# Kernel tuning notes

Hardware: AMD Instinct MI355X
Metric: run time of the kernel (lower is better)

The kernel has to match this reference:

```python
import jax, jax.numpy as jnp
import numpy as np

N = 100000
E = 1600000
IN_F = 256
OUT_F = 128
ALPHA = 0.2  # LeakyReLU negative slope


def setup_inputs() -> dict:
    key = jax.random.key(0)
    k_x, k_e, k_w, k_al, k_ar = jax.random.split(key, 5)
    x = jax.random.normal(k_x, (N, IN_F), dtype=jnp.float32)
    edge_index = jax.random.randint(k_e, (2, E), 0, N, dtype=jnp.int64)
    # xavier_uniform with gain=1.414
    gain = 1.414
    lim_w = gain * np.sqrt(6.0 / (IN_F + OUT_F))
    W = jax.random.uniform(k_w, (IN_F, OUT_F), dtype=jnp.float32, minval=-lim_w, maxval=lim_w)
    lim_a = gain * np.sqrt(6.0 / (OUT_F + 1))
    a_left = jax.random.uniform(k_al, (OUT_F, 1), dtype=jnp.float32, minval=-lim_a, maxval=lim_a)
    a_right = jax.random.uniform(k_ar, (OUT_F, 1), dtype=jnp.float32, minval=-lim_a, maxval=lim_a)
    return {"x": x, "edge_index": edge_index, "W": W, "a_left": a_left, "a_right": a_right}


def reference(x, edge_index, W, a_left, a_right):
    src = edge_index[0]  # destination of aggregation (rows of adj)
    dst = edge_index[1]  # neighbor being attended to
    Wh = x @ W                              # [N, out_f]
    e_left = (Wh @ a_left)[:, 0]            # [N]
    e_right = (Wh @ a_right)[:, 0]          # [N]
    e = e_left[src] + e_right[dst]          # [E]
    e = jnp.where(e > 0, e, ALPHA * e)      # LeakyReLU
    # segment softmax over edges grouped by src node
    e_max = jax.ops.segment_max(e, src, num_segments=N)          # [N]
    e_exp = jnp.exp(e - e_max[src])                               # [E]
    e_sum = jax.ops.segment_sum(e_exp, src, num_segments=N)       # [N]
    alpha = e_exp / (e_sum[src] + 1e-9)                           # [E]
    messages = alpha[:, None] * Wh[dst]                           # [E, out_f]
    output = jax.ops.segment_sum(messages, src, num_segments=N)   # [N, out_f]
    return jax.nn.relu(output)
```

## Files before the change

### kernel.cpp

```cpp
#include <hip/hip_runtime.h>
#include <cstdint>
#include <cstddef>

static constexpr int IN_F  = 256;
static constexpr int OUT_F = 128;
#define ALPHA_SLOPE 0.2f
#define NB 256
#define BUCK_SH 7
#define CAP 6144

typedef __attribute__((ext_vector_type(8))) short short8;
typedef __attribute__((ext_vector_type(4))) float f32x4;
union ABFrag { uint32_t u[4]; short8 v; };

__device__ __forceinline__ uint32_t pack_bf2(float lo, float hi) {
    uint32_t ul = __float_as_uint(lo), uh = __float_as_uint(hi);
    uint32_t rl = (ul + 0x7fffu + ((ul >> 16) & 1u)) >> 16;
    uint32_t rh = (uh + 0x7fffu + ((uh >> 16) & 1u)) & 0xffff0000u;
    return rl | rh;
}
__device__ __forceinline__ uint32_t cvtpk_bf2(float lo, float hi) {
    uint32_t r;
    asm("v_cvt_pk_bf16_f32 %0, %1, %2" : "=v"(r) : "v"(lo), "v"(hi));
    return r;
}
__device__ __forceinline__ float blo(uint32_t w) { return __uint_as_float(w << 16); }
__device__ __forceinline__ float bhi(uint32_t w) { return __uint_as_float(w & 0xffff0000u); }

#define RL_F(x, l) __uint_as_float(__builtin_amdgcn_readlane(__float_as_uint(x), (l)))
#define RL_I(x, l) __builtin_amdgcn_readlane((x), (l))

__device__ __forceinline__ int edge_at(const void* ei, int idx, int is64) {
    return is64 ? (int)((const long long*)ei)[idx] : ((const int*)ei)[idx];
}

__global__ __launch_bounds__(256) void prep_hist_kernel(
    const float* __restrict__ W, const float* __restrict__ aL,
    const float* __restrict__ aR, const void* __restrict__ EI,
    int E, int nbuk, uint32_t* __restrict__ WtH,
    float* __restrict__ waL, float* __restrict__ waR, int* __restrict__ C)
{
    if (blockIdx.x < 64) {
        int dd = blockIdx.x * 256 + threadIdx.x;
        int n  = dd >> 7;
        int kd = (dd & 127) ^ ((n & 7) << 2);
        int k  = kd * 2;
        WtH[dd] = pack_bf2(W[(size_t)k * OUT_F + n], W[(size_t)(k + 1) * OUT_F + n]);
        return;
    }
    if (blockIdx.x == 64) {
        int k = threadIdx.x;
        const float* wr = W + (size_t)k * OUT_F;
        float sl = 0.f, sr = 0.f;
        for (int j = 0; j < OUT_F; j++) {
            float wv = wr[j];
            sl = fmaf(wv, aL[j], sl);
            sr = fmaf(wv, aR[j], sr);
        }
        waL[k] = sl; waR[k] = sr;
        return;
    }
    __shared__ int h[800];
    __shared__ int det;
    if (threadIdx.x == 0) det = 0;
    for (int b = threadIdx.x; b < nbuk; b += 256) h[b] = 0;
    __syncthreads();
    {
        const unsigned* eu = (const unsigned*)EI;
        int nz = 0;
        for (int i = threadIdx.x; i < 1024; i += 256)
            if (eu[2 * i + 1] != 0u) nz++;
        if (nz) atomicAdd(&det, 1);
    }
    __syncthreads();
    const int is64 = (det == 0);
    const int bid = blockIdx.x - 65;
    int chunk = (E + NB - 1) / NB;
    int start = bid * chunk;
    int end = min(start + chunk, E);
    for (int i = start + threadIdx.x; i < end; i += 256) {
        int s = edge_at(EI, i, is64);
        atomicAdd(&h[s >> BUCK_SH], 1);
    }
    __syncthreads();
    for (int b = threadIdx.x; b < nbuk; b += 256)
        C[b * NB + bid] = h[b];
}

__global__ __launch_bounds__(256) void scan1_kernel(const int* __restrict__ counts,
                                                    int* __restrict__ offsets,
                                                    int* __restrict__ partials, int N) {
    __shared__ int wt[4];
    int gid = blockIdx.x * 256 + threadIdx.x;
    const int lane = threadIdx.x & 63, wave = threadIdx.x >> 6;
    int c = (gid < N) ? counts[gid] : 0;
    int incl = c;
#pragma unroll
    for (int o = 1; o < 64; o <<= 1) {
        int v = __shfl_up(incl, o);
        if (lane >= o) incl += v;
    }
    if (lane == 63) wt[wave] = incl;
    __syncthreads();
    int woff = 0;
    for (int w = 0; w < wave; w++) woff += wt[w];
    if (gid < N) offsets[gid] = woff + incl - c;
    if (threadIdx.x == 0) partials[blockIdx.x] = wt[0] + wt[1] + wt[2] + wt[3];
}

__global__ __launch_bounds__(256) void scan2_kernel(int* data, int n) {
    __shared__ int wt[4];
    __shared__ int carry_s;
    if (threadIdx.x == 0) carry_s = 0;
    __syncthreads();
    const int lane = threadIdx.x & 63, wave = threadIdx.x >> 6;
    for (int base = 0; base < n; base += 256) {
        int i = base + threadIdx.x;
        int c = (i < n) ? data[i] : 0;
        int incl = c;
#pragma unroll
        for (int o = 1; o < 64; o <<= 1) {
            int v = __shfl_up(incl, o);
            if (lane >= o) incl += v;
        }
        if (lane == 63) wt[wave] = incl;
        __syncthreads();
        int woff = 0;
        for (int w = 0; w < wave; w++) woff += wt[w];
        int total = wt[0] + wt[1] + wt[2] + wt[3];
        int carry = carry_s;
        __syncthreads();
        if (i < n) data[i] = carry + woff + incl - c;
        if (threadIdx.x == 0) carry_s = carry + total;
        __syncthreads();
    }
}

__global__ __launch_bounds__(512, 4) void gemm_scatter_kernel(
    const float* __restrict__ X, const uint32_t* __restrict__ WtH,
    const float* __restrict__ waL, const float* __restrict__ waR,
    uint32_t* __restrict__ Whh, float* __restrict__ el, float* __restrict__ er,
    int M, const void* __restrict__ EI, int E, int nbuk,
    const int* __restrict__ Cx, const int* __restrict__ T,
    uint32_t* __restrict__ entries, int GB)
{
    __shared__ uint32_t ldsW[16384];
    __shared__ int cur[800];
    __shared__ int det;
    const int tid = threadIdx.x;

    if (blockIdx.x >= GB) {
        if (tid == 0) det = 0;
        for (int b = tid; b < nbuk; b += 512) cur[b] = 0;
        __syncthreads();
        {
            const unsigned* eu = (const unsigned*)EI;
            int nz = 0;
            for (int i = tid; i < 1024; i += 512)
                if (eu[2 * i + 1] != 0u) nz++;
            if (nz) atomicAdd(&det, 1);
        }
        __syncthreads();
        const int is64 = (det == 0);
        const int bid = blockIdx.x - GB;
        int chunk = (E + NB - 1) / NB;
        int start = bid * chunk;
        int end = min(start + chunk, E);
        for (int i = start + tid; i < end; i += 512) {
            int s = edge_at(EI, i, is64);
            int d = edge_at(EI, E + i, is64);
            int b = s >> BUCK_SH;
            int pos = T[b] + Cx[b * NB + bid] + atomicAdd(&cur[b], 1);
            entries[pos] = ((uint32_t)(s & 127) << 17) | (uint32_t)d;
        }
        return;
    }

    const int w = tid >> 6, l = tid & 63;
    const int c = l & 15, kg = l >> 4;
    const int swz = (c & 7) << 2;

    {
        const uint4* src = (const uint4*)WtH;
        uint4* dst = (uint4*)ldsW;
#pragma unroll
        for (int i = 0; i < 8; i++)
            dst[tid + i * 512] = src[tid + i * 512];
    }

    const int bm = blockIdx.x * 128;
    const int myrow = w * 16 + c;
    const int grow = min(bm + myrow, M - 1);
    const bool rv = (bm + myrow) < M;
    const float* xp = X + (size_t)grow * IN_F + kg * 8;

    float4 xv[16];
#pragma unroll
    for (int ks = 0; ks < 8; ks++) {
        xv[2 * ks]     = *(const float4*)(xp + ks * 32);
        xv[2 * ks + 1] = *(const float4*)(xp + ks * 32 + 4);
    }

    f32x4 acc[8];
#pragma unroll
    for (int j = 0; j < 8; j++) acc[j] = (f32x4){0.f, 0.f, 0.f, 0.f};
    float sl = 0.f, sr = 0.f;

    __syncthreads();

#pragma unroll
    for (int ks = 0; ks < 8; ks++) {
        float4 xa = xv[2 * ks], xb = xv[2 * ks + 1];
        const float* wlp = waL + ks * 32 + kg * 8;
        const float* wrp = waR + ks * 32 + kg * 8;
        float4 l0 = *(const float4*)wlp, l1 = *(const float4*)(wlp + 4);
        float4 r0 = *(const float4*)wrp, r1 = *(const float4*)(wrp + 4);
        sl = fmaf(xa.x, l0.x, sl); sl = fmaf(xa.y, l0.y, sl);
        sl = fmaf(xa.z, l0.z, sl); sl = fmaf(xa.w, l0.w, sl);
        sl = fmaf(xb.x, l1.x, sl); sl = fmaf(xb.y, l1.y, sl);
        sl = fmaf(xb.z, l1.z, sl); sl = fmaf(xb.w, l1.w, sl);
        sr = fmaf(xa.x, r0.x, sr); sr = fmaf(xa.y, r0.y, sr);
        sr = fmaf(xa.z, r0.z, sr); sr = fmaf(xa.w, r0.w, sr);
        sr = fmaf(xb.x, r1.x, sr); sr = fmaf(xb.y, r1.y, sr);
        sr = fmaf(xb.z, r1.z, sr); sr = fmaf(xb.w, r1.w, sr);
        ABFrag a;
        a.u[0] = cvtpk_bf2(xa.x, xa.y); a.u[1] = cvtpk_bf2(xa.z, xa.w);
        a.u[2] = cvtpk_bf2(xb.x, xb.y); a.u[3] = cvtpk_bf2(xb.z, xb.w);
        const int kd = ks * 16 + kg * 4;
#pragma unroll
        for (int j = 0; j < 8; j++) {
            const int col = j * 16 + c;
            ABFrag b;
            *(uint4*)b.u = *(const uint4*)&ldsW[col * 128 + (kd ^ swz)];
            acc[j] = __builtin_amdgcn_mfma_f32_16x16x32_bf16(a.v, b.v, acc[j], 0, 0, 0);
        }
    }

    sl += __shfl_xor(sl, 16); sl += __shfl_xor(sl, 32);
    sr += __shfl_xor(sr, 16); sr += __shfl_xor(sr, 32);
    if (rv && kg == 0) { el[bm + myrow] = sl; er[bm + myrow] = sr; }

    __syncthreads();
    float* sc = (float*)ldsW + w * 2048;
#pragma unroll
    for (int j = 0; j < 8; j++)
#pragma unroll
        for (int r = 0; r < 4; r++)
            sc[(kg * 4 + r) * 128 + j * 16 + c] = acc[j][r];
    __syncthreads();
#pragma unroll
    for (int m = 0; m < 16; m++) {
        float2 p = *(const float2*)&sc[m * 128 + 2 * l];
        int orow = bm + w * 16 + m;
        if (orow < M) Whh[(size_t)orow * 64 + l] = cvtpk_bf2(p.x, p.y);
    }
}

__global__ __launch_bounds__(256) void bucket_kernel(const uint32_t* __restrict__ entries,
                                                     const int* __restrict__ T,
                                                     int E, int N, int nbuk,
                                                     int* __restrict__ offsets,
                                                     int* __restrict__ edge_dst) {
    __shared__ uint32_t ent[CAP];
    __shared__ int outD[CAP];
    __shared__ int cnt[128], pre[128], cur[128];
    __shared__ int wt4[2];
    const int b = blockIdx.x;
    const int tid = threadIdx.x;
    const int base = T[b];
    const int cend = (b + 1 < nbuk) ? T[b + 1] : E;
    int count = cend - base;
    if (count > CAP) count = CAP;

    if (tid < 128) { cnt[tid] = 0; cur[tid] = 0; }
    __syncthreads();
    for (int k = tid; k < count; k += 256) {
        uint32_t e = entries[base + k];
        ent[k] = e;
        atomicAdd(&cnt[e >> 17], 1);
    }
    __syncthreads();
    {
        const int lane = tid & 63, w = tid >> 6;
        int c = (tid < 128) ? cnt[tid] : 0;
        int incl = c;
#pragma unroll
        for (int o = 1; o < 64; o <<= 1) {
            int v = __shfl_up(incl, o);
            if (lane >= o) incl += v;
        }
        if (w == 0 && lane == 63) wt4[0] = incl;
        __syncthreads();
        if (tid < 128) pre[tid] = ((w == 1) ? wt4[0] : 0) + incl - c;
        __syncthreads();
    }
    const int node0 = b << BUCK_SH;
    const int nnode = min(128, N - node0);
    if (tid < nnode) offsets[node0 + tid] = base + pre[tid];
    if (b == nbuk - 1 && tid == 0) offsets[N] = E;
    for (int k = tid; k < count; k += 256) {
        uint32_t e = ent[k];
        int sl = e >> 17;
        int p = pre[sl] + atomicAdd(&cur[sl], 1);
        outD[p] = (int)(e & 0x1FFFFu);
    }
    __syncthreads();
    for (int k = tid; k < count; k += 256)
        edge_dst[base + k] = outD[k];
}

__global__ __launch_bounds__(256) void node_kernel(const int* __restrict__ offsets,
                                                   const int* __restrict__ edge_dst,
                                                   const float* __restrict__ el,
                                                   const float* __restrict__ er,
                                                   const uint32_t* __restrict__ WhH,
                                                   float* __restrict__ out, int N) {
    int node = blockIdx.x * 4 + (threadIdx.x >> 6);
    int lane = threadIdx.x & 63;
    if (node >= N) return;
    int s0  = offsets[node];
    int deg = offsets[node + 1] - s0;
    float eli = el[node];

    if (deg <= 64) {
        int dj = 0;
        float e = -3.402823466e38f;
        if (lane < deg) {
            dj = edge_dst[s0 + lane];
            float t = eli + er[dj];
            e = t > 0.f ? t : ALPHA_SLOPE * t;
        }
        float m = e;
#pragma unroll
        for (int o = 32; o > 0; o >>= 1) m = fmaxf(m, __shfl_xor(m, o));
        float ex = (lane < deg) ? expf(e - m) : 0.f;
        float ssum = ex;
#pragma unroll
        for (int o = 32; o > 0; o >>= 1) ssum += __shfl_xor(ssum, o);
        float p = ex / (ssum + 1e-9f);

        const int g = lane >> 4, q = lane & 15;
        float a0 = 0.f, a1 = 0.f, a2 = 0.f, a3 = 0.f;
        float a4 = 0.f, a5 = 0.f, a6 = 0.f, a7 = 0.f;
        int rounds = (deg + 3) >> 2;
        int r = 0;
        for (; r + 4 <= rounds; r += 4) {
            int i0 = (r << 2) + g, i1 = i0 + 4, i2 = i0 + 8, i3 = i0 + 12;
            float p0 = __shfl(p, i0), p1 = __shfl(p, i1);
            float p2 = __shfl(p, i2), p3 = __shfl(p, i3);
            int   e0 = __shfl(dj, i0), e1 = __shfl(dj, i1);
            int   e2 = __shfl(dj, i2), e3 = __shfl(dj, i3);
            uint4 w0 = *(const uint4*)&WhH[(size_t)e0 * 64 + q * 4];
            uint4 w1 = *(const uint4*)&WhH[(size_t)e1 * 64 + q * 4];
            uint4 w2 = *(const uint4*)&WhH[(size_t)e2 * 64 + q * 4];
            uint4 w3 = *(const uint4*)&WhH[(size_t)e3 * 64 + q * 4];
            a0 = fmaf(p0, blo(w0.x), a0); a1 = fmaf(p0, bhi(w0.x), a1);
            a2 = fmaf(p0, blo(w0.y), a2); a3 = fmaf(p0, bhi(w0.y), a3);
            a4 = fmaf(p0, blo(w0.z), a4); a5 = fmaf(p0, bhi(w0.z), a5);
            a6 = fmaf(p0, blo(w0.w), a6); a7 = fmaf(p0, bhi(w0.w), a7);
            a0 = fmaf(p1, blo(w1.x), a0); a1 = fmaf(p1, bhi(w1.x), a1);
            a2 = fmaf(p1, blo(w1.y), a2); a3 = fmaf(p1, bhi(w1.y), a3);
            a4 = fmaf(p1, blo(w1.z), a4); a5 = fmaf(p1, bhi(w1.z), a5);
            a6 = fmaf(p1, blo(w1.w), a6); a7 = fmaf(p1, bhi(w1.w), a7);
            a0 = fmaf(p2, blo(w2.x), a0); a1 = fmaf(p2, bhi(w2.x), a1);
            a2 = fmaf(p2, blo(w2.y), a2); a3 = fmaf(p2, bhi(w2.y), a3);
            a4 = fmaf(p2, blo(w2.z), a4); a5 = fmaf(p2, bhi(w2.z), a5);
            a6 = fmaf(p2, blo(w2.w), a6); a7 = fmaf(p2, bhi(w2.w), a7);
            a0 = fmaf(p3, blo(w3.x), a0); a1 = fmaf(p3, bhi(w3.x), a1);
            a2 = fmaf(p3, blo(w3.y), a2); a3 = fmaf(p3, bhi(w3.y), a3);
            a4 = fmaf(p3, blo(w3.z), a4); a5 = fmaf(p3, bhi(w3.z), a5);
            a6 = fmaf(p3, blo(w3.w), a6); a7 = fmaf(p3, bhi(w3.w), a7);
        }
        for (; r + 2 <= rounds; r += 2) {
            int i0 = (r << 2) + g, i1 = i0 + 4;
            float p0 = __shfl(p, i0), p1 = __shfl(p, i1);
            int   e0 = __shfl(dj, i0), e1 = __shfl(dj, i1);
            uint4 w0 = *(const uint4*)&WhH[(size_t)e0 * 64 + q * 4];
            uint4 w1 = *(const uint4*)&WhH[(size_t)e1 * 64 + q * 4];
            a0 = fmaf(p0, blo(w0.x), a0); a1 = fmaf(p0, bhi(w0.x), a1);
            a2 = fmaf(p0, blo(w0.y), a2); a3 = fmaf(p0, bhi(w0.y), a3);
            a4 = fmaf(p0, blo(w0.z), a4); a5 = fmaf(p0, bhi(w0.z), a5);
            a6 = fmaf(p0, blo(w0.w), a6); a7 = fmaf(p0, bhi(w0.w), a7);
            a0 = fmaf(p1, blo(w1.x), a0); a1 = fmaf(p1, bhi(w1.x), a1);
            a2 = fmaf(p1, blo(w1.y), a2); a3 = fmaf(p1, bhi(w1.y), a3);
            a4 = fmaf(p1, blo(w1.z), a4); a5 = fmaf(p1, bhi(w1.z), a5);
            a6 = fmaf(p1, blo(w1.w), a6); a7 = fmaf(p1, bhi(w1.w), a7);
        }
        if (r < rounds) {
            int i0 = (r << 2) + g;
            float p0 = __shfl(p, i0);
            int   e0 = __shfl(dj, i0);
            uint4 w0 = *(const uint4*)&WhH[(size_t)e0 * 64 + q * 4];
            a0 = fmaf(p0, blo(w0.x), a0); a1 = fmaf(p0, bhi(w0.x), a1);
            a2 = fmaf(p0, blo(w0.y), a2); a3 = fmaf(p0, bhi(w0.y), a3);
            a4 = fmaf(p0, blo(w0.z), a4); a5 = fmaf(p0, bhi(w0.z), a5);
            a6 = fmaf(p0, blo(w0.w), a6); a7 = fmaf(p0, bhi(w0.w), a7);
        }
#pragma unroll
        for (int o = 16; o <= 32; o <<= 1) {
            a0 += __shfl_xor(a0, o); a1 += __shfl_xor(a1, o);
            a2 += __shfl_xor(a2, o); a3 += __shfl_xor(a3, o);
            a4 += __shfl_xor(a4, o); a5 += __shfl_xor(a5, o);
            a6 += __shfl_xor(a6, o); a7 += __shfl_xor(a7, o);
        }
        if (g == 0) {
            float4 o0 = make_float4(fmaxf(a0, 0.f), fmaxf(a1, 0.f),
                                    fmaxf(a2, 0.f), fmaxf(a3, 0.f));
            float4 o1 = make_float4(fmaxf(a4, 0.f), fmaxf(a5, 0.f),
                                    fmaxf(a6, 0.f), fmaxf(a7, 0.f));
            float* op = out + (size_t)node * OUT_F + q * 8;
            *(float4*)op = o0;
            *(float4*)(op + 4) = o1;
        }
        return;
    }

    float m = -3.402823466e38f;
    for (int j = lane; j < deg; j += 64) {
        float e = eli + er[edge_dst[s0 + j]];
        e = e > 0.f ? e : ALPHA_SLOPE * e;
        m = fmaxf(m, e);
    }
#pragma unroll
    for (int o = 32; o > 0; o >>= 1) m = fmaxf(m, __shfl_xor(m, o));

    float ssum = 0.f;
    for (int j = lane; j < deg; j += 64) {
        float e = eli + er[edge_dst[s0 + j]];
        e = e > 0.f ? e : ALPHA_SLOPE * e;
        ssum += expf(e - m);
    }
#pragma unroll
    for (int o = 32; o > 0; o >>= 1) ssum += __shfl_xor(ssum, o);
    float inv = 1.f / (ssum + 1e-9f);

    float acc0 = 0.f, acc1 = 0.f;
    for (int base = 0; base < deg; base += 64) {
        int j = base + lane;
        float p = 0.f;
        int d = 0;
        if (j < deg) {
            d = edge_dst[s0 + j];
            float e = eli + er[d];
            e = e > 0.f ? e : ALPHA_SLOPE * e;
            p = expf(e - m) * inv;
        }
        int cnt = min(64, deg - base);
        int t = 0;
        for (; t + 8 <= cnt; t += 8) {
            float b0 = RL_F(p, t + 0), b1 = RL_F(p, t + 1);
            float b2 = RL_F(p, t + 2), b3 = RL_F(p, t + 3);
            float b4 = RL_F(p, t + 4), b5 = RL_F(p, t + 5);
            float b6 = RL_F(p, t + 6), b7 = RL_F(p, t + 7);
            int   d0 = RL_I(d, t + 0), d1 = RL_I(d, t + 1);
            int   d2 = RL_I(d, t + 2), d3 = RL_I(d, t + 3);
            int   d4 = RL_I(d, t + 4), d5 = RL_I(d, t + 5);
            int   d6 = RL_I(d, t + 6), d7 = RL_I(d, t + 7);
            uint32_t w0 = WhH[(size_t)d0 * 64 + lane];
            uint32_t w1 = WhH[(size_t)d1 * 64 + lane];
            uint32_t w2 = WhH[(size_t)d2 * 64 + lane];
            uint32_t w3 = WhH[(size_t)d3 * 64 + lane];
            uint32_t w4 = WhH[(size_t)d4 * 64 + lane];
            uint32_t w5 = WhH[(size_t)d5 * 64 + lane];
            uint32_t w6 = WhH[(size_t)d6 * 64 + lane];
            uint32_t w7 = WhH[(size_t)d7 * 64 + lane];
            acc0 = fmaf(b0, blo(w0), acc0); acc1 = fmaf(b0, bhi(w0), acc1);
            acc0 = fmaf(b1, blo(w1), acc0); acc1 = fmaf(b1, bhi(w1), acc1);
            acc0 = fmaf(b2, blo(w2), acc0); acc1 = fmaf(b2, bhi(w2), acc1);
            acc0 = fmaf(b3, blo(w3), acc0); acc1 = fmaf(b3, bhi(w3), acc1);
            acc0 = fmaf(b4, blo(w4), acc0); acc1 = fmaf(b4, bhi(w4), acc1);
            acc0 = fmaf(b5, blo(w5), acc0); acc1 = fmaf(b5, bhi(w5), acc1);
            acc0 = fmaf(b6, blo(w6), acc0); acc1 = fmaf(b6, bhi(w6), acc1);
            acc0 = fmaf(b7, blo(w7), acc0); acc1 = fmaf(b7, bhi(w7), acc1);
        }
        for (; t < cnt; ++t) {
            float a = RL_F(p, t);
            int  dd = RL_I(d, t);
            uint32_t wv = WhH[(size_t)dd * 64 + lane];
            acc0 = fmaf(a, blo(wv), acc0);
            acc1 = fmaf(a, bhi(wv), acc1);
        }
    }
    out[(size_t)node * OUT_F + 2 * lane]     = fmaxf(acc0, 0.f);
    out[(size_t)node * OUT_F + 2 * lane + 1] = fmaxf(acc1, 0.f);
}

extern "C" void kernel_launch(void* const* d_in, const int* in_sizes, int n_in,
                              void* d_out, int out_size, void* d_ws, size_t ws_size,
                              hipStream_t stream) {
    (void)n_in; (void)out_size; (void)ws_size;
    const float* X  = (const float*)d_in[0];
    const void*  EI = d_in[1];
    const float* W  = (const float*)d_in[2];
    const float* aL = (const float*)d_in[3];
    const float* aR = (const float*)d_in[4];
    float* out = (float*)d_out;
    const int N = in_sizes[0] / IN_F;
    const int E = in_sizes[1] / 2;
    const int nbuk = (N + 127) >> BUCK_SH;
    const int GB = (N + 127) / 128;

    char* ws = (char*)d_ws;
    float*    waL      = (float*)(ws + 256);
    float*    waR      = waL + 256;
    uint32_t* WtH      = (uint32_t*)(waR + 256);
    uint32_t* Whh      = WtH + 16384;
    float*    el       = (float*)(Whh + (size_t)N * 64);
    float*    er       = el + N;
    int*      T        = (int*)(er + N);
    int*      C        = T + 1024;
    int*      Cx       = C + (size_t)nbuk * NB;
    int*      offsets  = Cx + (size_t)nbuk * NB;
    uint32_t* entries  = (uint32_t*)(offsets + (N + 1));
    int*      edge_dst = (int*)(entries + E);

    prep_hist_kernel<<<65 + NB, 256, 0, stream>>>(W, aL, aR, EI, E, nbuk,
                                                  WtH, waL, waR, C);
    scan1_kernel<<<nbuk, 256, 0, stream>>>(C, Cx, T, nbuk * NB);
    scan2_kernel<<<1, 256, 0, stream>>>(T, nbuk);
    gemm_scatter_kernel<<<GB + NB, 512, 0, stream>>>(X, WtH, waL, waR, Whh, el, er,
                                                     N, EI, E, nbuk, Cx, T,
                                                     entries, GB);
    bucket_kernel<<<nbuk, 256, 0, stream>>>(entries, T, E, N, nbuk, offsets, edge_dst);
    node_kernel<<<(N + 3) / 4, 256, 0, stream>>>(offsets, edge_dst, el, er, Whh, out, N);
}
```

Measured before the change: 161.3 us.

## Stage weights via direct global-to-LDS loads and pipeline X loads with vmcnt waits

Replaces the register-staged copy of the bf16 weight matrix into LDS with global_load_lds direct transfers, and also stages the attention vectors into LDS. X row loads are issued as inline asm global_load_dwordx4 and consumed step by step with decreasing vmcnt waits, so MFMA work on early K-slices can overlap later loads. This relies on hand-counted vmcnt values and sched barriers; a wrong count or a compiler-inserted load would break correctness. Only one s_barrier is used before the LDS reads, which depends on vmcnt(16) covering the LDS-direct loads.

```diff
diff --git a/kernel.cpp b/kernel.cpp
--- a/kernel.cpp
+++ b/kernel.cpp
@@ -12,6 +12,9 @@
 typedef __attribute__((ext_vector_type(8))) short short8;
 typedef __attribute__((ext_vector_type(4))) float f32x4;
 union ABFrag { uint32_t u[4]; short8 v; };
+
+#define AS1 __attribute__((address_space(1)))
+#define AS3 __attribute__((address_space(3)))
 
 __device__ __forceinline__ uint32_t pack_bf2(float lo, float hi) {
     uint32_t ul = __float_as_uint(lo), uh = __float_as_uint(hi);
@@ -145,6 +148,7 @@
     uint32_t* __restrict__ entries, int GB)
 {
     __shared__ uint32_t ldsW[16384];
+    __shared__ float    ldsWA[512];
     __shared__ int cur[800];
     __shared__ int det;
     const int tid = threadIdx.x;
@@ -180,61 +184,80 @@
     const int c = l & 15, kg = l >> 4;
     const int swz = (c & 7) << 2;
 
-    {
-        const uint4* src = (const uint4*)WtH;
-        uint4* dst = (uint4*)ldsW;
-#pragma unroll
-        for (int i = 0; i < 8; i++)
-            dst[tid + i * 512] = src[tid + i * 512];
-    }
-
     const int bm = blockIdx.x * 128;
     const int myrow = w * 16 + c;
     const int grow = min(bm + myrow, M - 1);
     const bool rv = (bm + myrow) < M;
     const float* xp = X + (size_t)grow * IN_F + kg * 8;
 
-    float4 xv[16];
-#pragma unroll
-    for (int ks = 0; ks < 8; ks++) {
-        xv[2 * ks]     = *(const float4*)(xp + ks * 32);
-        xv[2 * ks + 1] = *(const float4*)(xp + ks * 32 + 4);
-    }
+    {
+        const float* wsrc = (tid < 256) ? (waL + tid) : (waR + (tid - 256));
+        __builtin_amdgcn_global_load_lds((AS1 const void*)wsrc,
+                                         (AS3 void*)&ldsWA[tid], 4, 0, 0);
+    }
+    {
+        const uint4* wsrc = (const uint4*)WtH;
+        uint4* wdst = (uint4*)ldsW;
+#pragma unroll
+        for (int i = 0; i < 8; i++)
+            __builtin_amdgcn_global_load_lds((AS1 const void*)(wsrc + tid + i * 512),
+                                             (AS3 void*)(wdst + tid + i * 512), 16, 0, 0);
+    }
+    __builtin_amdgcn_sched_barrier(0);
+
+    f32x4 xv[16];
+#define GLOAD(DST, OFFS) \
+    asm volatile("global_load_dwordx4 %0, %1, off offset:" OFFS : "=v"(DST) : "v"(xp))
+    GLOAD(xv[0],  "0");   GLOAD(xv[1],  "16");
+    GLOAD(xv[2],  "128"); GLOAD(xv[3],  "144");
+    GLOAD(xv[4],  "256"); GLOAD(xv[5],  "272");
+    GLOAD(xv[6],  "384"); GLOAD(xv[7],  "400");
+    GLOAD(xv[8],  "512"); GLOAD(xv[9],  "528");
+    GLOAD(xv[10], "640"); GLOAD(xv[11], "656");
+    GLOAD(xv[12], "768"); GLOAD(xv[13], "784");
+    GLOAD(xv[14], "896"); GLOAD(xv[15], "912");
+#undef GLOAD
+    __builtin_amdgcn_sched_barrier(0);
 
     f32x4 acc[8];
 #pragma unroll
     for (int j = 0; j < 8; j++) acc[j] = (f32x4){0.f, 0.f, 0.f, 0.f};
     float sl = 0.f, sr = 0.f;
 
-    __syncthreads();
-
-#pragma unroll
-    for (int ks = 0; ks < 8; ks++) {
-        float4 xa = xv[2 * ks], xb = xv[2 * ks + 1];
-        const float* wlp = waL + ks * 32 + kg * 8;
-        const float* wrp = waR + ks * 32 + kg * 8;
-        float4 l0 = *(const float4*)wlp, l1 = *(const float4*)(wlp + 4);
-        float4 r0 = *(const float4*)wrp, r1 = *(const float4*)(wrp + 4);
-        sl = fmaf(xa.x, l0.x, sl); sl = fmaf(xa.y, l0.y, sl);
-        sl = fmaf(xa.z, l0.z, sl); sl = fmaf(xa.w, l0.w, sl);
-        sl = fmaf(xb.x, l1.x, sl); sl = fmaf(xb.y, l1.y, sl);
-        sl = fmaf(xb.z, l1.z, sl); sl = fmaf(xb.w, l1.w, sl);
-        sr = fmaf(xa.x, r0.x, sr); sr = fmaf(xa.y, r0.y, sr);
-        sr = fmaf(xa.z, r0.z, sr); sr = fmaf(xa.w, r0.w, sr);
-        sr = fmaf(xb.x, r1.x, sr); sr = fmaf(xb.y, r1.y, sr);
-        sr = fmaf(xb.z, r1.z, sr); sr = fmaf(xb.w, r1.w, sr);
-        ABFrag a;
-        a.u[0] = cvtpk_bf2(xa.x, xa.y); a.u[1] = cvtpk_bf2(xa.z, xa.w);
-        a.u[2] = cvtpk_bf2(xb.x, xb.y); a.u[3] = cvtpk_bf2(xb.z, xb.w);
-        const int kd = ks * 16 + kg * 4;
-#pragma unroll
-        for (int j = 0; j < 8; j++) {
-            const int col = j * 16 + c;
-            ABFrag b;
-            *(uint4*)b.u = *(const uint4*)&ldsW[col * 128 + (kd ^ swz)];
-            acc[j] = __builtin_amdgcn_mfma_f32_16x16x32_bf16(a.v, b.v, acc[j], 0, 0, 0);
-        }
-    }
+    asm volatile("s_waitcnt vmcnt(16)");
+    __builtin_amdgcn_sched_barrier(0);
+    __builtin_amdgcn_s_barrier();
+    __builtin_amdgcn_sched_barrier(0);
+
+#define GSTEP(KS, VMS)                                                        \
+    {                                                                         \
+        asm volatile("s_waitcnt vmcnt(" VMS ")");                             \
+        __builtin_amdgcn_sched_barrier(0);                                    \
+        f32x4 xa = xv[2 * KS], xb = xv[2 * KS + 1];                           \
+        f32x4 l0 = *(const f32x4*)&ldsWA[KS * 32 + kg * 8];                   \
+        f32x4 l1 = *(const f32x4*)&ldsWA[KS * 32 + kg * 8 + 4];               \
+        f32x4 r0 = *(const f32x4*)&ldsWA[256 + KS * 32 + kg * 8];             \
+        f32x4 r1 = *(const f32x4*)&ldsWA[256 + KS * 32 + kg * 8 + 4];         \
+        _Pragma("unroll")                                                     \
+        for (int i = 0; i < 4; i++) {                                         \
+            sl = fmaf(xa[i], l0[i], sl); sl = fmaf(xb[i], l1[i], sl);         \
+            sr = fmaf(xa[i], r0[i], sr); sr = fmaf(xb[i], r1[i], sr);         \
+        }                                                                     \
+        ABFrag a;                                                             \
+        a.u[0] = cvtpk_bf2(xa[0], xa[1]); a.u[1] = cvtpk_bf2(xa[2], xa[3]);   \
+        a.u[2] = cvtpk_bf2(xb[0], xb[1]); a.u[3] = cvtpk_bf2(xb[2], xb[3]);   \
+        const int kd = KS * 16 + kg * 4;                                      \
+        _Pragma("unroll")                                                     \
+        for (int j = 0; j < 8; j++) {                                         \
+            const int col = j * 16 + c;                                       \
+            ABFrag b;                                                         \
+            *(uint4*)b.u = *(const uint4*)&ldsW[col * 128 + (kd ^ swz)];      \
+            acc[j] = __builtin_amdgcn_mfma_f32_16x16x32_bf16(a.v, b.v, acc[j], 0, 0, 0); \
+        }                                                                     \
+    }
+    GSTEP(0, "14"); GSTEP(1, "12"); GSTEP(2, "10"); GSTEP(3, "8");
+    GSTEP(4, "6");  GSTEP(5, "4");  GSTEP(6, "2");  GSTEP(7, "0");
+#undef GSTEP
 
     sl += __shfl_xor(sl, 16); sl += __shfl_xor(sl, 32);
     sr += __shfl_xor(sr, 16); sr += __shfl_xor(sr, 32);
```

After: 151.7 us (median of 2 runs). -5.9%, faster.
